# Kernel tuning notes

Hardware: AMD Instinct MI355X
Metric: run time of the kernel (lower is better)

The kernel has to match this reference:

```python
import jax, jax.numpy as jnp
import numpy as np

NUM_HEADS = 8
EPS = 1e-12  # torch F.normalize default eps


def setup_inputs() -> dict:
    key = jax.random.key(0)
    k0, k1, k2, k3 = jax.random.split(key, 4)
    b, c, d, h, w = 2, 64, 8, 128, 128
    x = jax.random.normal(k0, (b, c, d, h, w), dtype=jnp.float32)
    # 1x1x1 conv weights stored as [out, in]; depthwise 3x3x3 as [out, 1, kd, kh, kw]
    w_qkv = jax.random.normal(k1, (3 * c, c), dtype=jnp.float32) * 0.05
    w_dw = jax.random.normal(k2, (3 * c, 1, 3, 3, 3), dtype=jnp.float32) * 0.05
    temperature = jnp.ones((NUM_HEADS, 1, 1), dtype=jnp.float32)
    w_proj = jax.random.normal(k3, (c, c), dtype=jnp.float32) * 0.05
    return {"x": x, "w_qkv": w_qkv, "w_dw": w_dw, "temperature": temperature, "w_proj": w_proj}


def _l2norm(t):
    # F.normalize(t, dim=-1): t / max(||t||, eps)
    n = jnp.sqrt(jnp.sum(t * t, axis=-1, keepdims=True))
    return t / jnp.maximum(n, EPS)


def reference(x, w_qkv, w_dw, temperature, w_proj):
    b, c, d, h, w = x.shape
    heads = NUM_HEADS
    ch = c // heads  # per-head channel dim
    # 1x1x1 conv (pointwise) -> einsum over channels
    qkv = jnp.einsum('bcdhw,oc->bodhw', x, w_qkv)
    # depthwise 3x3x3 conv, padding 1 (SAME), groups = 3*c
    qkv = jax.lax.conv_general_dilated(
        qkv, w_dw, window_strides=(1, 1, 1), padding=[(1, 1)] * 3,
        feature_group_count=3 * c,
        dimension_numbers=('NCDHW', 'OIDHW', 'NCDHW'))
    q, k, v = jnp.split(qkv, 3, axis=1)
    n = d * h * w
    q = q.reshape(b, heads, ch, n)
    k = k.reshape(b, heads, ch, n)
    v = v.reshape(b, heads, ch, n)
    q = _l2norm(q)
    k = _l2norm(k)
    # channel-channel attention: [b, heads, ch, ch]
    attn = jnp.einsum('bhcn,bhen->bhce', q, k) * temperature
    attn = jax.nn.softmax(attn, axis=-1)
    out = jnp.einsum('bhce,bhen->bhcn', attn, v)
    out = out.reshape(b, c, d, h, w)
    out = jnp.einsum('bcdhw,oc->bodhw', out, w_proj)
    return out
```

## Files before the change

kernel.cpp:

```cpp
#include <hip/hip_runtime.h>
#include <math.h>

#define NPOS 131072
#define GC 128

typedef __attribute__((ext_vector_type(8))) short short8v;
typedef __attribute__((ext_vector_type(4))) float f32x4;

__device__ __forceinline__ size_t baddr(int b, int c, int p) {
  return ((size_t)(b * 2048 + (p >> 6)) * 64 + c) * 64 + (p & 63);
}

__device__ __forceinline__ void bf16split(float x, unsigned short& hi, unsigned short& lo) {
  unsigned u = __float_as_uint(x);
  hi = (unsigned short)(u >> 16);
  float hif = __uint_as_float(u & 0xffff0000u);
  float l = x - hif;
  lo = (unsigned short)(__float_as_uint(l) >> 16);
}

__global__ void k_prep(const float* __restrict__ w_qkv, unsigned short* __restrict__ whi,
                       unsigned short* __restrict__ wlo) {
  int idx = blockIdx.x * 256 + threadIdx.x;
  if (idx < 12288) {
    int j = idx & 7, l = (idx >> 3) & 63, ks = (idx >> 9) & 1, ot = (idx >> 10) & 3,
        g = idx >> 12;
    int out = ot * 16 + (l & 15);
    int k = ks * 32 + (l >> 4) * 8 + j;
    bf16split(w_qkv[(g * 64 + out) * 64 + k], whi[idx], wlo[idx]);
  }
}

__device__ __forceinline__ void pw_mfma_core(float (*xl)[66], const short8v (*ahi)[2],
                                             const short8v (*alo)[2], int tid) {
  const int lane = tid & 63;
  const int wid = tid >> 6;
  const int prow = lane & 15, kgrp = lane >> 4;
  const int pos = wid * 16 + prow;
  short8v bh[2], bl[2];
#pragma unroll
  for (int ks = 0; ks < 2; ++ks)
#pragma unroll
    for (int j = 0; j < 8; ++j) {
      unsigned short h, lo16;
      bf16split(xl[ks * 32 + kgrp * 8 + j][pos], h, lo16);
      bh[ks][j] = (short)h;
      bl[ks][j] = (short)lo16;
    }
  f32x4 D[4];
#pragma unroll
  for (int ot = 0; ot < 4; ++ot) {
    f32x4 d = {0.f, 0.f, 0.f, 0.f};
#pragma unroll
    for (int ks = 0; ks < 2; ++ks) {
      d = __builtin_amdgcn_mfma_f32_16x16x32_bf16(ahi[ot][ks], bh[ks], d, 0, 0, 0);
      d = __builtin_amdgcn_mfma_f32_16x16x32_bf16(ahi[ot][ks], bl[ks], d, 0, 0, 0);
      d = __builtin_amdgcn_mfma_f32_16x16x32_bf16(alo[ot][ks], bh[ks], d, 0, 0, 0);
    }
    D[ot] = d;
  }
  __syncthreads();
#pragma unroll
  for (int ot = 0; ot < 4; ++ot)
#pragma unroll
    for (int jj = 0; jj < 4; ++jj)
      xl[ot * 16 + kgrp * 4 + jj][pos] = D[ot][jj];
  __syncthreads();
}

__global__ __launch_bounds__(256) void k_pw_mfma(const float* __restrict__ x,
                                                 const unsigned short* __restrict__ whi,
                                                 const unsigned short* __restrict__ wlo,
                                                 float* __restrict__ pre) {
  const int id = blockIdx.x;
  const int sid = (id & 7) * 512 + (id >> 3);
  const int b = sid >> 11;
  const int t = sid & 2047;
  const int p0 = t * 64;
  const int lane = threadIdx.x & 63;
  const int tid = threadIdx.x;
  const int f4 = tid & 15;
  __shared__ __align__(16) float xl[64][66];
  short8v ahi[4][2], alo[4][2];
#pragma unroll
  for (int ot = 0; ot < 4; ++ot)
#pragma unroll
    for (int ks = 0; ks < 2; ++ks) {
      int fi = ((ot * 2 + ks) * 64 + lane) * 8;
      ahi[ot][ks] = *(const short8v*)&whi[fi];
      alo[ot][ks] = *(const short8v*)&wlo[fi];
    }
  const float* xb = x + ((size_t)b * 64) * NPOS + p0;
#pragma unroll
  for (int r = 0; r < 4; ++r) {
    int ch2 = (r * 256 + tid) >> 4;
    *(float4*)&xl[ch2][f4 * 4] = *(const float4*)&xb[(size_t)ch2 * NPOS + f4 * 4];
  }
  __syncthreads();
  pw_mfma_core(xl, ahi, alo, tid);
  float* go = pre + ((size_t)(b * 2048 + t) * 64) * 64;
#pragma unroll
  for (int r = 0; r < 4; ++r) {
    int idx = r * 256 + tid;
    *(float4*)&go[(size_t)idx * 4] = *(const float4*)&xl[idx >> 4][(idx & 15) * 4];
  }
}

__global__ __launch_bounds__(256) void k_dw(const float* __restrict__ pre,
                                            const float* __restrict__ w_dw,
                                            float* __restrict__ conv,
                                            float* __restrict__ nsq, int g) {
  const int id = blockIdx.x;
  const int sid = (id & 7) * 1024 + (id >> 3);
  const int z = sid >> 6, r = sid & 63, by = r >> 2, bx = r & 3;
  const int b = z >> 6;
  const int c = z & 63;
  const int h0 = by * 8;
  const int w0 = bx * 32;
  __shared__ float t[10][10][40];
  __shared__ float red[4];
  const int tid = threadIdx.y * 32 + threadIdx.x;
  for (int i = tid; i < 800; i += 256) {
    int j = i & 7, row = i >> 3;
    int h = row % 10, dpl = row / 10;
    int dd = dpl - 1, hh = h0 + h - 1;
    float4 v = make_float4(0.f, 0.f, 0.f, 0.f);
    if (dd >= 0 && dd < 8 && hh >= 0 && hh < 128) {
      int p = dd * 16384 + hh * 128 + w0 + j * 4;
      v = *(const float4*)&pre[baddr(b, c, p)];
    }
    *(float4*)&t[dpl][h][4 + j * 4] = v;
  }
  for (int i = tid; i < 200; i += 256) {
    int side = i & 1, row = i >> 1;
    int h = row % 10, dpl = row / 10;
    int dd = dpl - 1, hh = h0 + h - 1;
    int ww = side ? (w0 + 32) : (w0 - 1);
    float v = 0.f;
    if (dd >= 0 && dd < 8 && hh >= 0 && hh < 128 && ww >= 0 && ww < 128)
      v = pre[baddr(b, c, dd * 16384 + hh * 128 + ww)];
    t[dpl][h][side ? 36 : 3] = v;
  }
  float wk[27];
#pragma unroll
  for (int i = 0; i < 27; ++i) wk[i] = w_dw[(g * 64 + c) * 27 + i];
  __syncthreads();
  const int wl = threadIdx.x, hl = threadIdx.y;
  float acc[8];
#pragma unroll
  for (int d = 0; d < 8; ++d) acc[d] = 0.f;
#pragma unroll
  for (int dpl = 0; dpl < 10; ++dpl)
#pragma unroll
    for (int kh = 0; kh < 3; ++kh)
#pragma unroll
      for (int kw = 0; kw < 3; ++kw) {
        float f = t[dpl][hl + kh][3 + wl + kw];
#pragma unroll
        for (int kd = 0; kd < 3; ++kd) {
          const int d = dpl - kd;
          if (d >= 0 && d < 8)
            acc[d] = fmaf(f, wk[(kd * 3 + kh) * 3 + kw], acc[d]);
        }
      }
  float nsum = 0.f;
#pragma unroll
  for (int d = 0; d < 8; ++d) {
    int p = d * 16384 + (h0 + hl) * 128 + (w0 + wl);
    conv[baddr(b, c, p)] = acc[d];
    nsum = fmaf(acc[d], acc[d], nsum);
  }
  if (nsq) {
    const int lane = tid & 63, wv = tid >> 6;
    float v = nsum;
    v += __shfl_down(v, 32); v += __shfl_down(v, 16); v += __shfl_down(v, 8);
    v += __shfl_down(v, 4);  v += __shfl_down(v, 2);  v += __shfl_down(v, 1);
    if (lane == 0) red[wv] = v;
    __syncthreads();
    if (tid == 0) {
      const int blk = by * 4 + bx;
      nsq[((size_t)b * 64 + c) * 64 + blk] = red[0] + red[1] + red[2] + red[3];
    }
  }
}

__global__ __launch_bounds__(256) void k_gramS(const float* __restrict__ qconv,
                                               const float* __restrict__ kconv,
                                               float* __restrict__ partialS) {
  const int chunk = blockIdx.x;
  const int bh = blockIdx.y;
  const int b = bh >> 3, head = bh & 7;
  const int tid = threadIdx.x;
  const int c0 = head * 8;
  float S[64];
#pragma unroll
  for (int i = 0; i < 64; ++i) S[i] = 0.f;
#pragma unroll
  for (int it = 0; it < 4; ++it) {
    int p = chunk * 1024 + it * 256 + tid;
    size_t tbase = ((size_t)(b * 2048 + (p >> 6)) * 64) * 64 + (p & 63);
    float qv[8], kv[8];
#pragma unroll
    for (int c = 0; c < 8; ++c) qv[c] = qconv[tbase + (size_t)(c0 + c) * 64];
#pragma unroll
    for (int e = 0; e < 8; ++e) kv[e] = kconv[tbase + (size_t)(c0 + e) * 64];
#pragma unroll
    for (int c = 0; c < 8; ++c)
#pragma unroll
      for (int e = 0; e < 8; ++e) S[c * 8 + e] = fmaf(qv[c], kv[e], S[c * 8 + e]);
  }
#pragma unroll
  for (int i = 0; i < 64; ++i) asm volatile("" : "+v"(S[i]));

  const int lane = tid & 63, wv = tid >> 6;
#define BSTEP(src, dst, n, s)                                        \
  {                                                                  \
    const bool hi_ = (lane >> (s)) & 1;                              \
    _Pragma("unroll")                                                \
    for (int i_ = 0; i_ < (n); ++i_) {                               \
      float send_ = hi_ ? src[i_] : src[i_ + (n)];                   \
      float mine_ = hi_ ? src[i_ + (n)] : src[i_];                   \
      dst[i_] = mine_ + __shfl_xor(send_, 1 << (s));                 \
    }                                                                \
  }
  float v32[32], v16[16], v8[8], v4[4], v2[2], v1[1];
  BSTEP(S,   v32, 32, 0)
  BSTEP(v32, v16, 16, 1)
  BSTEP(v16, v8,   8, 2)
  BSTEP(v8,  v4,   4, 3)
  BSTEP(v4,  v2,   2, 4)
  BSTEP(v2,  v1,   1, 5)
#undef BSTEP
  const int idx = ((lane & 1) << 5) | ((lane & 2) << 3) | ((lane & 4) << 1) |
                  ((lane & 8) >> 1) | ((lane & 16) >> 3) | ((lane & 32) >> 5);
  __shared__ float red[4][64];
  red[wv][idx] = v1[0];
  __syncthreads();
  if (tid < 64) {
    float s = red[0][tid] + red[1][tid] + red[2][tid] + red[3][tid];
    partialS[((size_t)bh * GC + chunk) * 64 + tid] = s;
  }
}

__global__ void k_attn(const float* __restrict__ partialS, const float* __restrict__ nqp,
                       const float* __restrict__ nkp, const float* __restrict__ temp,
                       float* __restrict__ A) {
  const int bh = blockIdx.x;
  const int b = bh >> 3, head = bh & 7;
  const int tid = threadIdx.x;
  __shared__ float sums[80];
  if (tid < 64) {
    float s = 0.f;
    const float* pp = partialS + (size_t)bh * GC * 64 + tid;
    for (int j = 0; j < GC; ++j) s += pp[j * 64];
    sums[tid] = s;
  } else if (tid < 72) {
    const int e = tid - 64;
    float s = 0.f;
    const float* pp = nkp + ((size_t)b * 64 + head * 8 + e) * 64;
    for (int j = 0; j < 64; ++j) s += pp[j];
    sums[64 + e] = s;
  } else if (tid < 80) {
    const int c = tid - 72;
    float s = 0.f;
    const float* pp = nqp + ((size_t)b * 64 + head * 8 + c) * 64;
    for (int j = 0; j < 64; ++j) s += pp[j];
    sums[72 + c] = s;
  }
  __syncthreads();
  if (tid < 8) {
    const int c = tid;
    float tp = temp[head];
    float qd = fmaxf(sqrtf(sums[72 + c]), 1e-12f);
    float vals[8];
    float mx = -1e30f;
#pragma unroll
    for (int e = 0; e < 8; ++e) {
      float kd = fmaxf(sqrtf(sums[64 + e]), 1e-12f);
      vals[e] = sums[c * 8 + e] / (qd * kd) * tp;
      mx = fmaxf(mx, vals[e]);
    }
    float den = 0.f;
#pragma unroll
    for (int e = 0; e < 8; ++e) { vals[e] = expf(vals[e] - mx); den += vals[e]; }
#pragma unroll
    for (int e = 0; e < 8; ++e) A[bh * 64 + c * 8 + e] = vals[e] / den;
  }
}

__global__ void k_M(const float* __restrict__ w_proj, const float* __restrict__ A,
                    unsigned short* __restrict__ Mhi, unsigned short* __restrict__ Mlo) {
  const int b = blockIdx.x;
  for (int e = threadIdx.x; e < 4096; e += 256) {
    int j = e & 7, l = (e >> 3) & 63, ks = (e >> 9) & 1, ot = (e >> 10) & 3;
    int out = ot * 16 + (l & 15);
    int gch = ks * 32 + (l >> 4) * 8 + j;
    int hg = gch >> 3, jj = gch & 7;
    float s = 0.f;
#pragma unroll
    for (int i = 0; i < 8; ++i)
      s += w_proj[out * 64 + hg * 8 + i] * A[(b * 8 + hg) * 64 + i * 8 + jj];
    bf16split(s, Mhi[b * 4096 + e], Mlo[b * 4096 + e]);
  }
}

__global__ __launch_bounds__(256) void k_out_mfma(const float* __restrict__ vconv,
                                                  const unsigned short* __restrict__ Mhi,
                                                  const unsigned short* __restrict__ Mlo,
                                                  float* __restrict__ out) {
  const int id = blockIdx.x;
  const int sid = (id & 7) * 512 + (id >> 3);
  const int b = sid >> 11;
  const int t = sid & 2047;
  const int p0 = t * 64;
  const int lane = threadIdx.x & 63;
  const int tid = threadIdx.x;
  const int f4 = tid & 15;
  __shared__ __align__(16) float xl[64][66];
  short8v ahi[4][2], alo[4][2];
#pragma unroll
  for (int ot = 0; ot < 4; ++ot)
#pragma unroll
    for (int ks = 0; ks < 2; ++ks) {
      int fi = b * 4096 + ((ot * 2 + ks) * 64 + lane) * 8;
      ahi[ot][ks] = *(const short8v*)&Mhi[fi];
      alo[ot][ks] = *(const short8v*)&Mlo[fi];
    }
  const float* gi = vconv + ((size_t)(b * 2048 + t) * 64) * 64;
#pragma unroll
  for (int r = 0; r < 4; ++r) {
    int idx = r * 256 + tid;
    *(float4*)&xl[idx >> 4][(idx & 15) * 4] = *(const float4*)&gi[(size_t)idx * 4];
  }
  __syncthreads();
  pw_mfma_core(xl, ahi, alo, tid);
  float* ob = out + ((size_t)b * 64) * NPOS + p0;
#pragma unroll
  for (int r = 0; r < 4; ++r) {
    int row = (r * 256 + tid) >> 4;
    *(float4*)&ob[(size_t)row * NPOS + f4 * 4] = *(const float4*)&xl[row][f4 * 4];
  }
}

extern "C" void kernel_launch(void* const* d_in, const int* in_sizes, int n_in,
                              void* d_out, int out_size, void* d_ws, size_t ws_size,
                              hipStream_t stream) {
  const float* x      = (const float*)d_in[0];
  const float* w_qkv  = (const float*)d_in[1];
  const float* w_dw   = (const float*)d_in[2];
  const float* temp   = (const float*)d_in[3];
  const float* w_proj = (const float*)d_in[4];
  float* out = (float*)d_out;
  float* ws  = (float*)d_ws;

  float* conv_buf = ws;
  float* kconv    = conv_buf + 16777216ull;
  float* nqp      = kconv + 16777216ull;
  float* nkp      = nqp + 8192ull;
  float* partialS = nkp + 8192ull;
  float* Abuf     = partialS + 131072ull;
  unsigned short* whi = (unsigned short*)(Abuf + 1024ull);
  unsigned short* wlo = whi + 12288ull;
  unsigned short* Mhi = wlo + 12288ull;
  unsigned short* Mlo = Mhi + 8192ull;

  k_prep<<<48, 256, 0, stream>>>(w_qkv, whi, wlo);
  k_pw_mfma<<<4096, 256, 0, stream>>>(x, whi, wlo, out);
  k_dw<<<8192, dim3(32, 8), 0, stream>>>(out, w_dw, conv_buf, nqp, 0);
  k_pw_mfma<<<4096, 256, 0, stream>>>(x, whi + 4096, wlo + 4096, out);
  k_dw<<<8192, dim3(32, 8), 0, stream>>>(out, w_dw, kconv, nkp, 1);
  k_gramS<<<dim3(GC, 16), 256, 0, stream>>>(conv_buf, kconv, partialS);
  k_attn<<<16, 128, 0, stream>>>(partialS, nqp, nkp, temp, Abuf);
  k_M<<<2, 256, 0, stream>>>(w_proj, Abuf, Mhi, Mlo);
  k_pw_mfma<<<4096, 256, 0, stream>>>(x, whi + 8192, wlo + 8192, out);
  k_dw<<<8192, dim3(32, 8), 0, stream>>>(out, w_dw, conv_buf, nullptr, 2);
  k_out_mfma<<<4096, 256, 0, stream>>>(conv_buf, Mhi, Mlo, out);
}
```

Baseline: 234.5 us.

## Switch intermediate layout to full-row 128-wide tiles and widen depthwise tiles

The intermediate channel-blocked layout changes from 64-position tiles to full 128-wide W rows, so each pointwise block now handles 128 positions and writes contiguous rows. The depthwise conv block now covers whole W rows for 4 H rows, which removes the separate W-halo loads and their scattered single-float reads. It also halves the number of blocks for all kernels and updates the gram, norm-partial and attention indexing to match. The cost is more shared memory and registers per block (two MFMA halves held in registers, a larger LDS tile), which may lower occupancy.

```diff
diff --git a/kernel.cpp b/kernel.cpp
--- a/kernel.cpp
+++ b/kernel.cpp
@@ -7,9 +7,6 @@
 typedef __attribute__((ext_vector_type(8))) short short8v;
 typedef __attribute__((ext_vector_type(4))) float f32x4;
 
-__device__ __forceinline__ size_t baddr(int b, int c, int p) {
-  return ((size_t)(b * 2048 + (p >> 6)) * 64 + c) * 64 + (p & 63);
-}
 
 __device__ __forceinline__ void bf16split(float x, unsigned short& hi, unsigned short& lo) {
   unsigned u = __float_as_uint(x);
@@ -31,40 +28,47 @@
   }
 }
 
-__device__ __forceinline__ void pw_mfma_core(float (*xl)[66], const short8v (*ahi)[2],
+__device__ __forceinline__ void pw_mfma_core(float (*xl)[136], const short8v (*ahi)[2],
                                              const short8v (*alo)[2], int tid) {
   const int lane = tid & 63;
   const int wid = tid >> 6;
   const int prow = lane & 15, kgrp = lane >> 4;
-  const int pos = wid * 16 + prow;
-  short8v bh[2], bl[2];
-#pragma unroll
-  for (int ks = 0; ks < 2; ++ks)
-#pragma unroll
-    for (int j = 0; j < 8; ++j) {
-      unsigned short h, lo16;
-      bf16split(xl[ks * 32 + kgrp * 8 + j][pos], h, lo16);
-      bh[ks][j] = (short)h;
-      bl[ks][j] = (short)lo16;
-    }
-  f32x4 D[4];
-#pragma unroll
-  for (int ot = 0; ot < 4; ++ot) {
-    f32x4 d = {0.f, 0.f, 0.f, 0.f};
-#pragma unroll
-    for (int ks = 0; ks < 2; ++ks) {
-      d = __builtin_amdgcn_mfma_f32_16x16x32_bf16(ahi[ot][ks], bh[ks], d, 0, 0, 0);
-      d = __builtin_amdgcn_mfma_f32_16x16x32_bf16(ahi[ot][ks], bl[ks], d, 0, 0, 0);
-      d = __builtin_amdgcn_mfma_f32_16x16x32_bf16(alo[ot][ks], bh[ks], d, 0, 0, 0);
-    }
-    D[ot] = d;
-  }
-  __syncthreads();
-#pragma unroll
-  for (int ot = 0; ot < 4; ++ot)
-#pragma unroll
-    for (int jj = 0; jj < 4; ++jj)
-      xl[ot * 16 + kgrp * 4 + jj][pos] = D[ot][jj];
+  f32x4 D[2][4];
+#pragma unroll
+  for (int half = 0; half < 2; ++half) {
+    const int pos = half * 64 + wid * 16 + prow;
+    short8v bh[2], bl[2];
+#pragma unroll
+    for (int ks = 0; ks < 2; ++ks)
+#pragma unroll
+      for (int j = 0; j < 8; ++j) {
+        unsigned short h, lo16;
+        bf16split(xl[ks * 32 + kgrp * 8 + j][pos], h, lo16);
+        bh[ks][j] = (short)h;
+        bl[ks][j] = (short)lo16;
+      }
+#pragma unroll
+    for (int ot = 0; ot < 4; ++ot) {
+      f32x4 d = {0.f, 0.f, 0.f, 0.f};
+#pragma unroll
+      for (int ks = 0; ks < 2; ++ks) {
+        d = __builtin_amdgcn_mfma_f32_16x16x32_bf16(ahi[ot][ks], bh[ks], d, 0, 0, 0);
+        d = __builtin_amdgcn_mfma_f32_16x16x32_bf16(ahi[ot][ks], bl[ks], d, 0, 0, 0);
+        d = __builtin_amdgcn_mfma_f32_16x16x32_bf16(alo[ot][ks], bh[ks], d, 0, 0, 0);
+      }
+      D[half][ot] = d;
+    }
+  }
+  __syncthreads();
+#pragma unroll
+  for (int half = 0; half < 2; ++half) {
+    const int pos = half * 64 + wid * 16 + prow;
+#pragma unroll
+    for (int ot = 0; ot < 4; ++ot)
+#pragma unroll
+      for (int jj = 0; jj < 4; ++jj)
+        xl[ot * 16 + kgrp * 4 + jj][pos] = D[half][ot][jj];
+  }
   __syncthreads();
 }
 
@@ -73,14 +77,13 @@
                                                  const unsigned short* __restrict__ wlo,
                                                  float* __restrict__ pre) {
   const int id = blockIdx.x;
-  const int sid = (id & 7) * 512 + (id >> 3);
-  const int b = sid >> 11;
-  const int t = sid & 2047;
-  const int p0 = t * 64;
+  const int sid = (id & 7) * 256 + (id >> 3);
+  const int b = sid >> 10;
+  const int t = sid & 1023;
+  const int p0 = t * 128;
   const int lane = threadIdx.x & 63;
   const int tid = threadIdx.x;
-  const int f4 = tid & 15;
-  __shared__ __align__(16) float xl[64][66];
+  __shared__ __align__(16) float xl[64][136];
   short8v ahi[4][2], alo[4][2];
 #pragma unroll
   for (int ot = 0; ot < 4; ++ot)
@@ -92,17 +95,18 @@
     }
   const float* xb = x + ((size_t)b * 64) * NPOS + p0;
 #pragma unroll
-  for (int r = 0; r < 4; ++r) {
-    int ch2 = (r * 256 + tid) >> 4;
-    *(float4*)&xl[ch2][f4 * 4] = *(const float4*)&xb[(size_t)ch2 * NPOS + f4 * 4];
+  for (int r = 0; r < 8; ++r) {
+    int idx = r * 256 + tid;
+    int ch = idx >> 5, j = idx & 31;
+    *(float4*)&xl[ch][j * 4] = *(const float4*)&xb[(size_t)ch * NPOS + j * 4];
   }
   __syncthreads();
   pw_mfma_core(xl, ahi, alo, tid);
-  float* go = pre + ((size_t)(b * 2048 + t) * 64) * 64;
-#pragma unroll
-  for (int r = 0; r < 4; ++r) {
+  float* go = pre + (size_t)(b * 1024 + t) * 8192;
+#pragma unroll
+  for (int r = 0; r < 8; ++r) {
     int idx = r * 256 + tid;
-    *(float4*)&go[(size_t)idx * 4] = *(const float4*)&xl[idx >> 4][(idx & 15) * 4];
+    *(float4*)&go[(size_t)idx * 4] = *(const float4*)&xl[idx >> 5][(idx & 31) * 4];
   }
 }
 
@@ -111,64 +115,59 @@
                                             float* __restrict__ conv,
                                             float* __restrict__ nsq, int g) {
   const int id = blockIdx.x;
-  const int sid = (id & 7) * 1024 + (id >> 3);
-  const int z = sid >> 6, r = sid & 63, by = r >> 2, bx = r & 3;
-  const int b = z >> 6;
-  const int c = z & 63;
-  const int h0 = by * 8;
-  const int w0 = bx * 32;
-  __shared__ float t[10][10][40];
+  const int sid = (id & 7) * 512 + (id >> 3);
+  const int b = sid >> 11;
+  const int c = (sid >> 5) & 63;
+  const int hg = sid & 31;
+  const int h0 = hg * 4;
+  __shared__ float t[10][6][136];
   __shared__ float red[4];
-  const int tid = threadIdx.y * 32 + threadIdx.x;
-  for (int i = tid; i < 800; i += 256) {
-    int j = i & 7, row = i >> 3;
-    int h = row % 10, dpl = row / 10;
+  const int tid = threadIdx.x;
+  for (int i = tid; i < 180; i += 256) {
+    int row = i / 3, e = i - row * 3;
+    int dpl = row / 6, h = row - dpl * 6;
+    t[dpl][h][e == 0 ? 3 : 131 + e] = 0.f;
+  }
+  for (int i = tid; i < 1920; i += 256) {
+    int dpl = i / 192, rem = i - dpl * 192;
+    int h = rem >> 5, j = rem & 31;
     int dd = dpl - 1, hh = h0 + h - 1;
     float4 v = make_float4(0.f, 0.f, 0.f, 0.f);
-    if (dd >= 0 && dd < 8 && hh >= 0 && hh < 128) {
-      int p = dd * 16384 + hh * 128 + w0 + j * 4;
-      v = *(const float4*)&pre[baddr(b, c, p)];
-    }
+    if (dd >= 0 && dd < 8 && hh >= 0 && hh < 128)
+      v = *(const float4*)&pre[((size_t)((b * 1024 + dd * 128 + hh) * 64 + c)) * 128 + j * 4];
     *(float4*)&t[dpl][h][4 + j * 4] = v;
   }
-  for (int i = tid; i < 200; i += 256) {
-    int side = i & 1, row = i >> 1;
-    int h = row % 10, dpl = row / 10;
-    int dd = dpl - 1, hh = h0 + h - 1;
-    int ww = side ? (w0 + 32) : (w0 - 1);
-    float v = 0.f;
-    if (dd >= 0 && dd < 8 && hh >= 0 && hh < 128 && ww >= 0 && ww < 128)
-      v = pre[baddr(b, c, dd * 16384 + hh * 128 + ww)];
-    t[dpl][h][side ? 36 : 3] = v;
-  }
   float wk[27];
 #pragma unroll
   for (int i = 0; i < 27; ++i) wk[i] = w_dw[(g * 64 + c) * 27 + i];
   __syncthreads();
-  const int wl = threadIdx.x, hl = threadIdx.y;
-  float acc[8];
-#pragma unroll
-  for (int d = 0; d < 8; ++d) acc[d] = 0.f;
-#pragma unroll
-  for (int dpl = 0; dpl < 10; ++dpl)
-#pragma unroll
-    for (int kh = 0; kh < 3; ++kh)
-#pragma unroll
-      for (int kw = 0; kw < 3; ++kw) {
-        float f = t[dpl][hl + kh][3 + wl + kw];
-#pragma unroll
-        for (int kd = 0; kd < 3; ++kd) {
-          const int d = dpl - kd;
-          if (d >= 0 && d < 8)
-            acc[d] = fmaf(f, wk[(kd * 3 + kh) * 3 + kw], acc[d]);
+  const int w = tid & 127, h2 = tid >> 7;
+  float nsum = 0.f;
+#pragma unroll
+  for (int hh2 = 0; hh2 < 2; ++hh2) {
+    const int hl = h2 + hh2 * 2;
+    float acc[8];
+#pragma unroll
+    for (int d = 0; d < 8; ++d) acc[d] = 0.f;
+#pragma unroll
+    for (int dpl = 0; dpl < 10; ++dpl)
+#pragma unroll
+      for (int kh = 0; kh < 3; ++kh)
+#pragma unroll
+        for (int kw = 0; kw < 3; ++kw) {
+          float f = t[dpl][hl + kh][3 + w + kw];
+#pragma unroll
+          for (int kd = 0; kd < 3; ++kd) {
+            const int d = dpl - kd;
+            if (d >= 0 && d < 8)
+              acc[d] = fmaf(f, wk[(kd * 3 + kh) * 3 + kw], acc[d]);
+          }
         }
-      }
-  float nsum = 0.f;
-#pragma unroll
-  for (int d = 0; d < 8; ++d) {
-    int p = d * 16384 + (h0 + hl) * 128 + (w0 + wl);
-    conv[baddr(b, c, p)] = acc[d];
-    nsum = fmaf(acc[d], acc[d], nsum);
+#pragma unroll
+    for (int d = 0; d < 8; ++d) {
+      conv[((size_t)((b * 1024 + d * 128 + h0 + hl) * 64 + c)) * 128 + w] = acc[d];
+      nsum = fmaf(acc[d], acc[d], nsum);
+    }
   }
   if (nsq) {
     const int lane = tid & 63, wv = tid >> 6;
@@ -177,10 +176,8 @@
     v += __shfl_down(v, 4);  v += __shfl_down(v, 2);  v += __shfl_down(v, 1);
     if (lane == 0) red[wv] = v;
     __syncthreads();
-    if (tid == 0) {
-      const int blk = by * 4 + bx;
-      nsq[((size_t)b * 64 + c) * 64 + blk] = red[0] + red[1] + red[2] + red[3];
-    }
+    if (tid == 0)
+      nsq[((size_t)b * 64 + c) * 32 + hg] = red[0] + red[1] + red[2] + red[3];
   }
 }
 
@@ -198,12 +195,13 @@
 #pragma unroll
   for (int it = 0; it < 4; ++it) {
     int p = chunk * 1024 + it * 256 + tid;
-    size_t tbase = ((size_t)(b * 2048 + (p >> 6)) * 64) * 64 + (p & 63);
+    int d = p >> 14, h = (p >> 7) & 127, w = p & 127;
+    size_t base = ((size_t)((b * 1024 + d * 128 + h) * 64 + c0)) * 128 + w;
     float qv[8], kv[8];
 #pragma unroll
-    for (int c = 0; c < 8; ++c) qv[c] = qconv[tbase + (size_t)(c0 + c) * 64];
-#pragma unroll
-    for (int e = 0; e < 8; ++e) kv[e] = kconv[tbase + (size_t)(c0 + e) * 64];
+    for (int c = 0; c < 8; ++c) qv[c] = qconv[base + (size_t)c * 128];
+#pragma unroll
+    for (int e = 0; e < 8; ++e) kv[e] = kconv[base + (size_t)e * 128];
 #pragma unroll
     for (int c = 0; c < 8; ++c)
 #pragma unroll
@@ -257,14 +255,14 @@
   } else if (tid < 72) {
     const int e = tid - 64;
     float s = 0.f;
-    const float* pp = nkp + ((size_t)b * 64 + head * 8 + e) * 64;
-    for (int j = 0; j < 64; ++j) s += pp[j];
+    const float* pp = nkp + ((size_t)b * 64 + head * 8 + e) * 32;
+    for (int j = 0; j < 32; ++j) s += pp[j];
     sums[64 + e] = s;
   } else if (tid < 80) {
     const int c = tid - 72;
     float s = 0.f;
-    const float* pp = nqp + ((size_t)b * 64 + head * 8 + c) * 64;
-    for (int j = 0; j < 64; ++j) s += pp[j];
+    const float* pp = nqp + ((size_t)b * 64 + head * 8 + c) * 32;
+    for (int j = 0; j < 32; ++j) s += pp[j];
     sums[72 + c] = s;
   }
   __syncthreads();
@@ -309,14 +307,13 @@
                                                   const unsigned short* __restrict__ Mlo,
                                                   float* __restrict__ out) {
   const int id = blockIdx.x;
-  const int sid = (id & 7) * 512 + (id >> 3);
-  const int b = sid >> 11;
-  const int t = sid & 2047;
-  const int p0 = t * 64;
+  const int sid = (id & 7) * 256 + (id >> 3);
+  const int b = sid >> 10;
+  const int t = sid & 1023;
+  const int p0 = t * 128;
   const int lane = threadIdx.x & 63;
   const int tid = threadIdx.x;
-  const int f4 = tid & 15;
-  __shared__ __align__(16) float xl[64][66];
+  __shared__ __align__(16) float xl[64][136];
   short8v ahi[4][2], alo[4][2];
 #pragma unroll
   for (int ot = 0; ot < 4; ++ot)
@@ -326,19 +323,20 @@
       ahi[ot][ks] = *(const short8v*)&Mhi[fi];
       alo[ot][ks] = *(const short8v*)&Mlo[fi];
     }
-  const float* gi = vconv + ((size_t)(b * 2048 + t) * 64) * 64;
-#pragma unroll
-  for (int r = 0; r < 4; ++r) {
+  const float* gi = vconv + (size_t)(b * 1024 + t) * 8192;
+#pragma unroll
+  for (int r = 0; r < 8; ++r) {
     int idx = r * 256 + tid;
-    *(float4*)&xl[idx >> 4][(idx & 15) * 4] = *(const float4*)&gi[(size_t)idx * 4];
+    *(float4*)&xl[idx >> 5][(idx & 31) * 4] = *(const float4*)&gi[(size_t)idx * 4];
   }
   __syncthreads();
   pw_mfma_core(xl, ahi, alo, tid);
   float* ob = out + ((size_t)b * 64) * NPOS + p0;
 #pragma unroll
-  for (int r = 0; r < 4; ++r) {
-    int row = (r * 256 + tid) >> 4;
-    *(float4*)&ob[(size_t)row * NPOS + f4 * 4] = *(const float4*)&xl[row][f4 * 4];
+  for (int r = 0; r < 8; ++r) {
+    int idx = r * 256 + tid;
+    int o = idx >> 5, j = idx & 31;
+    *(float4*)&ob[(size_t)o * NPOS + j * 4] = *(const float4*)&xl[o][j * 4];
   }
 }
 
@@ -365,14 +363,14 @@
   unsigned short* Mlo = Mhi + 8192ull;
 
   k_prep<<<48, 256, 0, stream>>>(w_qkv, whi, wlo);
-  k_pw_mfma<<<4096, 256, 0, stream>>>(x, whi, wlo, out);
-  k_dw<<<8192, dim3(32, 8), 0, stream>>>(out, w_dw, conv_buf, nqp, 0);
-  k_pw_mfma<<<4096, 256, 0, stream>>>(x, whi + 4096, wlo + 4096, out);
-  k_dw<<<8192, dim3(32, 8), 0, stream>>>(out, w_dw, kconv, nkp, 1);
+  k_pw_mfma<<<2048, 256, 0, stream>>>(x, whi, wlo, out);
+  k_dw<<<4096, 256, 0, stream>>>(out, w_dw, conv_buf, nqp, 0);
+  k_pw_mfma<<<2048, 256, 0, stream>>>(x, whi + 4096, wlo + 4096, out);
+  k_dw<<<4096, 256, 0, stream>>>(out, w_dw, kconv, nkp, 1);
   k_gramS<<<dim3(GC, 16), 256, 0, stream>>>(conv_buf, kconv, partialS);
   k_attn<<<16, 128, 0, stream>>>(partialS, nqp, nkp, temp, Abuf);
   k_M<<<2, 256, 0, stream>>>(w_proj, Abuf, Mhi, Mlo);
-  k_pw_mfma<<<4096, 256, 0, stream>>>(x, whi + 8192, wlo + 8192, out);
-  k_dw<<<8192, dim3(32, 8), 0, stream>>>(out, w_dw, conv_buf, nullptr, 2);
-  k_out_mfma<<<4096, 256, 0, stream>>>(conv_buf, Mhi, Mlo, out);
-}
+  k_pw_mfma<<<2048, 256, 0, stream>>>(x, whi + 8192, wlo + 8192, out);
+  k_dw<<<4096, 256, 0, stream>>>(out, w_dw, conv_buf, nullptr, 2);
+  k_out_mfma<<<2048, 256, 0, stream>>>(conv_buf, Mhi, Mlo, out);
+}
```

Result: no change. 232.4 us (-0.9%).
